# Optimization experiments

Measured on AMD Instinct MI355X. Metric: run time of the kernel, lower is better.

Reference implementation:

```python
import jax, jax.numpy as jnp
import numpy as np

H, W, S, B = 256, 256, 16, 8  # dim=(H,W); S hardcoded in forward; B = 1 + events[-1,-1]
N = 4_000_000


def _shift2d(a, dy, dx):
    """Replicates F.pad(a, (pad(dx) + pad(dy)))[:H,:W] where pad(n)=(n,0) if n>=0 else (0,-n).
    Positive diff shifts content right/down and zero-fills; negative diff is a no-op
    (right/bottom padding followed by top-left crop is identity)."""
    sy = jnp.maximum(dy, 0)
    sx = jnp.maximum(dx, 0)
    a = jnp.roll(a, shift=(sy, sx), axis=(0, 1))
    row = jnp.arange(a.shape[0])[:, None]
    col = jnp.arange(a.shape[1])[None, :]
    return jnp.where((row >= sy) & (col >= sx), a, 0.0)


def setup_inputs():
    key = jax.random.key(0)
    k1, k2, k3, k4 = jax.random.split(key, 4)
    x = jax.random.randint(k1, (N,), 0, W).astype(jnp.float32)
    y = jax.random.randint(k2, (N,), 0, H).astype(jnp.float32)
    t = jax.random.uniform(k3, (N,), minval=1e-3, maxval=1.0)
    p = (jax.random.randint(k4, (N,), 0, 2) * 2 - 1).astype(jnp.float32)
    b = jnp.repeat(jnp.arange(B, dtype=jnp.float32), N // B)  # sorted so events[-1,-1]==B-1
    events = jnp.stack([x, y, t, p, b], axis=1)
    return {"events": events}


def _forward(events):
    x = events[:, 0]
    y = events[:, 1]
    t = events[:, 2]
    bi = events[:, 4].astype(jnp.int32)

    # per-batch time normalization: t /= max(t) within each sample
    t_max = jax.ops.segment_max(t, bi, num_segments=B)
    t = t / t_max[bi]

    xi = x.astype(jnp.int32)
    yi = y.astype(jnp.int32)

    # container: per-pixel event count histogram, (B,H,W)
    idx_c = xi + W * yi + W * H * bi
    container = jnp.zeros(B * H * W, jnp.int32).at[idx_c].add(1).reshape(B, H, W)

    # time_segment[e] = number of thresholds i/S (i=1..S-1) with t >= i/S
    thr = jnp.arange(1, S, dtype=t.dtype) / S
    ts = jnp.searchsorted(thr, t, side='right').astype(jnp.int32)

    # combiner accumulates the segment index itself (as in the torch code)
    idx_cb = xi + W * yi + W * H * ts + W * H * S * bi
    combiner = jnp.zeros(B * S * H * W, jnp.int32).at[idx_cb].add(ts)
    combiner = combiner.reshape(B, S, H, W).astype(jnp.float32)

    # per-(batch, segment) event counts and x/y centroids
    seg = bi * S + ts
    cnt = jax.ops.segment_sum(jnp.ones_like(t), seg, num_segments=B * S).reshape(B, S)
    xm = jax.ops.segment_sum(x, seg, num_segments=B * S).reshape(B, S) / cnt
    ym = jax.ops.segment_sum(y, seg, num_segments=B * S).reshape(B, S) / cnt

    # mean-shift alignment + accumulation of the S segment images
    combined = []
    for b_ in range(B):
        segment = combiner[b_, 0]
        x_mean = xm[b_, 0]
        y_mean = ym[b_, 0]
        pts = cnt[b_, 0]  # note: never updated in the original code
        for i in range(1, S):
            cond = cnt[b_, i] > pts
            tmp = jnp.where(cond, segment, combiner[b_, i])
            base = jnp.where(cond, combiner[b_, i], segment)
            dx = jnp.floor(jnp.where(cond, xm[b_, i] - x_mean, x_mean - xm[b_, i])).astype(jnp.int32)
            dy = jnp.floor(jnp.where(cond, ym[b_, i] - y_mean, y_mean - ym[b_, i])).astype(jnp.int32)
            x_mean = jnp.where(cond, xm[b_, i], x_mean)
            y_mean = jnp.where(cond, ym[b_, i], y_mean)
            segment = base + _shift2d(tmp, dy, dx)
        combined.append(jax.nn.relu(segment - S))
    combined_img = jnp.stack(combined)  # (B,H,W)

    # half-resolution count + mean-timestamp voxel grids
    hw4 = (H // 2) * (W // 2)
    idx_ct = xi // 2 + (W // 2) * (yi // 2) + (W * H * bi) // 4
    counter = jnp.zeros(B * hw4, jnp.int32).at[idx_ct].add(1).astype(jnp.float32)
    divider = jnp.where(counter == 0, 1.0, counter)
    timer = jnp.zeros(B * hw4, jnp.float32).at[idx_ct].add(t) / divider
    counter = counter.reshape(B, H // 2, W // 2)
    timer = timer.reshape(B, H // 2, W // 2)

    # 2x2 difference pooling of the count image
    dyv = container[:, ::2] - container[:, 1::2]
    dyv = (dyv[:, :, ::2] + dyv[:, :, 1::2]).astype(jnp.float32)
    dxv = container[:, :, ::2] - container[:, :, 1::2]
    dxv = (dxv[:, 1::2] + dxv[:, ::2]).astype(jnp.float32)

    # F.interpolate(scale_factor=0.5, mode='nearest') == ::2 subsampling for even H,W
    combined_half = combined_img[:, ::2, ::2]

    return jnp.stack([dxv, dyv, timer, counter, combined_half], axis=1)  # (B,5,H/2,W/2)


def reference(events):
    return _forward(events)
```

## Files before the change

kernel.cpp:

```cpp
#include <hip/hip_runtime.h>

#define SS 16
#define BB 8
#define CHUNKS 32

#define OFF_CNT    0
#define OFF_XS     512
#define OFF_YS     1024
#define OFF_BMAX   1536
#define OFF_P4REP  5632
#define OFF_CMREP  (5632 + 16777216)
#define OFF_XYREC  (5632 + 16777216 + 8388608)
#define OFF_TARR   (5632 + 16777216 + 8388608 + 8000000)
#define OFF_TSREC  (5632 + 16777216 + 8388608 + 8000000 + 16000000)


__global__ void k_prep(const float4* __restrict__ ev4, int nq, unsigned* __restrict__ bmax,
                       uint2* __restrict__ xyrec, float4* __restrict__ tarr,
                       int* __restrict__ cnt, int* __restrict__ xs, int* __restrict__ ys) {
    if (blockIdx.x == 0 && threadIdx.x < BB * SS) {
        cnt[threadIdx.x] = 0; xs[threadIdx.x] = 0; ys[threadIdx.x] = 0;
    }
    int bb = blockIdx.x >> 7;
    long base = (long)bb * nq;
    unsigned m = 0;
    for (int q = (blockIdx.x & 127) * blockDim.x + threadIdx.x; q < nq; q += 128 * blockDim.x) {
        const float4* p = ev4 + (base + q) * 5;
        float4 f0 = p[0], f1 = p[1], f2 = p[2], f3 = p[3], f4 = p[4];
        unsigned xy0 = (unsigned)(int)f0.x | ((unsigned)(int)f0.y << 8)
                     | ((unsigned)(int)f1.y << 16) | ((unsigned)(int)f1.z << 24);
        unsigned xy1 = (unsigned)(int)f2.z | ((unsigned)(int)f2.w << 8)
                     | ((unsigned)(int)f3.w << 16) | ((unsigned)(int)f4.x << 24);
        xyrec[base + q] = make_uint2(xy0, xy1);
        tarr[base + q]  = make_float4(f0.z, f1.w, f3.x, f4.y);
        unsigned t0 = __float_as_uint(f0.z), t1 = __float_as_uint(f1.w);
        unsigned t2 = __float_as_uint(f3.x), t3 = __float_as_uint(f4.y);
        unsigned a = t0 > t1 ? t0 : t1;
        unsigned b2 = t2 > t3 ? t2 : t3;
        a = a > b2 ? a : b2;
        m = m > a ? m : a;
    }
    #pragma unroll
    for (int off = 32; off; off >>= 1) {
        unsigned o = (unsigned)__shfl_xor((int)m, off, 64);
        m = m > o ? m : o;
    }
    __shared__ unsigned sm;
    if (threadIdx.x == 0) sm = 0;
    __syncthreads();
    if ((threadIdx.x & 63) == 0) atomicMax(&sm, m);
    __syncthreads();
    if (threadIdx.x == 0) bmax[blockIdx.x] = sm;
}

__global__ void __launch_bounds__(1024, 8)
k_main(const uint2* __restrict__ xyrec, const float4* __restrict__ tarr, int nq,
       const unsigned* __restrict__ bmax,
       unsigned* __restrict__ p4rep, unsigned short* __restrict__ tsrec,
       int* __restrict__ cnt, int* __restrict__ xs, int* __restrict__ ys) {
    __shared__ unsigned p4s[16384];
    __shared__ unsigned long long stat[SS * 8];
    __shared__ unsigned stmax;
    int bb = blockIdx.x >> 5;
    int ch = blockIdx.x & 31;
    if (threadIdx.x == 0) stmax = 0u;
    if (threadIdx.x < SS * 8) stat[threadIdx.x] = 0ull;
    for (int i = threadIdx.x; i < 16384; i += 1024) p4s[i] = 0u;
    __syncthreads();
    if (threadIdx.x < 128) atomicMax(&stmax, bmax[bb * 128 + threadIdx.x]);
    __syncthreads();
    float tm = __uint_as_float(stmax);
    long base = (long)bb * nq;
    int slot = threadIdx.x & 7;
    for (int q = ch * 1024 + threadIdx.x; q < nq; q += CHUNKS * 1024) {
        uint2 xy = xyrec[base + q];
        float4 t4 = tarr[base + q];
        float T[4] = { t4.x, t4.y, t4.z, t4.w };
        unsigned XY[4] = { xy.x & 0xFFFFu, xy.x >> 16, xy.y & 0xFFFFu, xy.y >> 16 };
        unsigned tsn = 0;
        #pragma unroll
        for (int k = 0; k < 4; k++) {
            int xi = (int)(XY[k] & 255u), yi = (int)(XY[k] >> 8);
            float tn = __fdiv_rn(T[k], tm);
            int ts = (int)(tn * 16.0f);
            if (ts > 15) ts = 15;
            unsigned qfix = __float2uint_rn(tn * 256.0f);
            unsigned v = qfix | (1u << 14)
                | (((unsigned)(xi & 1) ^ 1u) << 20)
                | (((unsigned)(yi & 1) ^ 1u) << 26);
            atomicAdd(&p4s[((yi >> 1) << 7) + (xi >> 1)], v);
            atomicAdd(&stat[ts * 8 + slot], 1ull | ((unsigned long long)xi << 20)
                                                 | ((unsigned long long)yi << 42));
            tsn |= (unsigned)ts << (4 * k);
        }
        tsrec[base + q] = (unsigned short)tsn;
    }
    __syncthreads();
    unsigned* dst = p4rep + (long)blockIdx.x * 16384;
    for (int i = threadIdx.x; i < 16384; i += 1024) dst[i] = p4s[i];
    if (threadIdx.x < SS) {
        unsigned long long v = 0ull;
        #pragma unroll
        for (int s = 0; s < 8; s++) v += stat[threadIdx.x * 8 + s];
        if (v) {
            int g = bb * SS + threadIdx.x;
            atomicAdd(&cnt[g], (int)(v & 0xFFFFF));
            atomicAdd(&xs[g],  (int)((v >> 20) & 0x3FFFFF));
            atomicAdd(&ys[g],  (int)(v >> 42));
        }
    }
}

__global__ void __launch_bounds__(1024, 8)
k_comb(const uint2* __restrict__ xyrec, const unsigned short* __restrict__ tsrec, int nq,
       const int* __restrict__ cnt, const int* __restrict__ xs, const int* __restrict__ ys,
       const unsigned* __restrict__ p4rep,
       unsigned* __restrict__ cmrep32, float* __restrict__ out) {
    __shared__ int combs[16384];
    __shared__ double xm[SS], ym[SS];
    __shared__ int cs[SS], ssy[SS], ssx[SS];
    int bb = blockIdx.x >> 5;
    int ch = blockIdx.x & 31;
    for (int i = threadIdx.x; i < 16384; i += 1024) combs[i] = 0;
    if (threadIdx.x < SS) {
        int g = bb * SS + threadIdx.x;
        int cc = cnt[g];
        cs[threadIdx.x] = cc;
        xm[threadIdx.x] = (double)xs[g] / (double)cc;
        ym[threadIdx.x] = (double)ys[g] / (double)cc;
    }
    __syncthreads();
    if (threadIdx.x == 0) {
        double x_mean = xm[0], y_mean = ym[0];
        int c0 = cs[0];
        int sy[SS], sx[SS];
        for (int k = 0; k < SS; k++) { sy[k] = 0; sx[k] = 0; }
        for (int k = 1; k < SS; k++) {
            bool cond = cs[k] > c0;
            double ddx = cond ? (xm[k] - x_mean) : (x_mean - xm[k]);
            double ddy = cond ? (ym[k] - y_mean) : (y_mean - ym[k]);
            int dx = (int)floor(ddx);
            int dy = (int)floor(ddy);
            int px = dx > 0 ? dx : 0;
            int py = dy > 0 ? dy : 0;
            if (cond) {
                for (int j = 0; j < k; j++) { sy[j] += py; sx[j] += px; }
                x_mean = xm[k]; y_mean = ym[k];
            } else {
                sy[k] = py; sx[k] = px;
            }
        }
        for (int k = 0; k < SS; k++) { ssy[k] = sy[k]; ssx[k] = sx[k]; }
    }
    __syncthreads();
    long base = (long)bb * nq;
    for (int q = ch * 1024 + threadIdx.x; q < nq; q += CHUNKS * 1024) {
        uint2 xy = xyrec[base + q];
        unsigned tsn = tsrec[base + q];
        unsigned XY[4] = { xy.x & 0xFFFFu, xy.x >> 16, xy.y & 0xFFFFu, xy.y >> 16 };
        #pragma unroll
        for (int k = 0; k < 4; k++) {
            int ts = (int)((tsn >> (4 * k)) & 15u);
            if (ts) {
                int yy = (int)(XY[k] >> 8) + ssy[ts];
                int xx = (int)(XY[k] & 255u) + ssx[ts];
                if (yy < 256 && xx < 256 && !((yy | xx) & 1))
                    atomicAdd(&combs[((yy >> 1) << 7) + (xx >> 1)], ts);
            }
        }
    }
    __syncthreads();
    unsigned* dst = cmrep32 + (long)blockIdx.x * 8192;
    for (int i = threadIdx.x; i < 8192; i += 1024)
        dst[i] = (unsigned)combs[2 * i] | ((unsigned)combs[2 * i + 1] << 16);
    if (threadIdx.x < 512) {
        int lin = blockIdx.x * 512 + threadIdx.x;
        int hp = lin & 16383;
        int b  = lin >> 14;
        long rb = (long)b * CHUNKS * 16384 + hp;
        unsigned tfix = 0; int c = 0, Ex = 0, Ey = 0;
        #pragma unroll 8
        for (int r = 0; r < CHUNKS; r++) {
            unsigned v = p4rep[rb + (long)r * 16384];
            tfix += v & 0x3FFFu;
            c    += (int)((v >> 14) & 63u);
            Ex   += (int)((v >> 20) & 63u);
            Ey   += (int)(v >> 26);
        }
        float tsum = (float)tfix * (1.0f / 256.0f);
        float ctr = (float)c;
        int obase = (b * 5) << 14;
        out[obase             + hp] = (float)(2 * Ex - c);
        out[obase +     16384 + hp] = (float)(2 * Ey - c);
        out[obase + 2 * 16384 + hp] = tsum / (c == 0 ? 1.0f : ctr);
        out[obase + 3 * 16384 + hp] = ctr;
    }
}

__global__ void k_out(const unsigned short* __restrict__ cmrep,
                      float* __restrict__ out) {
    int lin = blockIdx.x * blockDim.x + threadIdx.x;
    int hp = lin & 16383;
    int b  = lin >> 14;
    long rb = (long)b * CHUNKS * 16384 + hp;
    int cm = 0;
    #pragma unroll 8
    for (int r = 0; r < CHUNKS; r++) cm += cmrep[rb + (long)r * 16384];
    float cmb = (float)cm - 16.0f;
    cmb = cmb < 0.0f ? 0.0f : cmb;
    out[((b * 5 + 4) << 14) + hp] = cmb;
}

extern "C" void kernel_launch(void* const* d_in, const int* in_sizes, int n_in,
                              void* d_out, int out_size, void* d_ws, size_t ws_size,
                              hipStream_t stream) {
    const float4* ev4 = (const float4*)d_in[0];
    int n  = in_sizes[0] / 5;
    int nb = n / BB;
    int nq = nb / 4;
    char* ws = (char*)d_ws;
    int*      cnt   = (int*)     (ws + OFF_CNT);
    int*      xs    = (int*)     (ws + OFF_XS);
    int*      ys    = (int*)     (ws + OFF_YS);
    unsigned* bmax  = (unsigned*)(ws + OFF_BMAX);
    unsigned* p4rep = (unsigned*)(ws + OFF_P4REP);
    unsigned* cmrep32 = (unsigned*)(ws + OFF_CMREP);
    uint2*    xyrec = (uint2*)   (ws + OFF_XYREC);
    float4*   tarr  = (float4*)  (ws + OFF_TARR);
    unsigned short* tsrec = (unsigned short*)(ws + OFF_TSREC);

    hipLaunchKernelGGL(k_prep, dim3(1024), dim3(256),  0, stream, ev4, nq, bmax,
                       xyrec, tarr, cnt, xs, ys);
    hipLaunchKernelGGL(k_main, dim3(256),  dim3(1024), 0, stream, xyrec, tarr, nq,
                       bmax, p4rep, tsrec, cnt, xs, ys);
    hipLaunchKernelGGL(k_comb, dim3(256),  dim3(1024), 0, stream, xyrec, tsrec, nq,
                       cnt, xs, ys, p4rep, cmrep32, (float*)d_out);
    hipLaunchKernelGGL(k_out,  dim3(128),  dim3(1024), 0, stream,
                       (const unsigned short*)cmrep32, (float*)d_out);
}
```

Measured before the change: 139.7 us.

## Fuse four kernels into one cooperative kernel with grid syncs and LDS-resident records

Replaces the prep, main, combine and output kernels with a single cooperative launch of 256 blocks that separates phases with grid.sync(). Packed xy coordinates and per-event segment indices now stay in shared memory across phases instead of round-tripping through global workspace, and the p4s buffer is reused as the combiner histogram. This removes three kernel launches and about 8 MB of global traffic, at the cost of grid-wide barrier overhead and more LDS per block (about 100 KB), which limits residency to one 1024-thread block per CU.

```diff
diff --git a/kernel.cpp b/kernel.cpp
--- a/kernel.cpp
+++ b/kernel.cpp
@@ -1,4 +1,7 @@
 #include <hip/hip_runtime.h>
+#include <hip/hip_cooperative_groups.h>
+
+namespace cg = cooperative_groups;
 
 #define SS 16
 #define BB 8
@@ -10,127 +13,122 @@
 #define OFF_BMAX   1536
 #define OFF_P4REP  5632
 #define OFF_CMREP  (5632 + 16777216)
-#define OFF_XYREC  (5632 + 16777216 + 8388608)
-#define OFF_TARR   (5632 + 16777216 + 8388608 + 8000000)
-#define OFF_TSREC  (5632 + 16777216 + 8388608 + 8000000 + 16000000)
-
-
-__global__ void k_prep(const float4* __restrict__ ev4, int nq, unsigned* __restrict__ bmax,
-                       uint2* __restrict__ xyrec, float4* __restrict__ tarr,
-                       int* __restrict__ cnt, int* __restrict__ xs, int* __restrict__ ys) {
-    if (blockIdx.x == 0 && threadIdx.x < BB * SS) {
-        cnt[threadIdx.x] = 0; xs[threadIdx.x] = 0; ys[threadIdx.x] = 0;
-    }
-    int bb = blockIdx.x >> 7;
-    long base = (long)bb * nq;
+#define OFF_TARR   (5632 + 16777216 + 8388608)
+
+
+__global__ void __launch_bounds__(1024)
+k_fused(const float4* __restrict__ ev4, int nq, unsigned* __restrict__ bmax,
+        float4* __restrict__ tarr, unsigned* __restrict__ p4rep,
+        unsigned* __restrict__ cmrep32, int* __restrict__ cnt,
+        int* __restrict__ xs, int* __restrict__ ys, float* __restrict__ out) {
+    cg::grid_group grid = cg::this_grid();
+    __shared__ unsigned p4s[16384];
+    __shared__ uint2 xyl[4096];
+    __shared__ unsigned short tsl[4096];
+    __shared__ unsigned long long stat[SS * 8];
+    __shared__ unsigned stmax;
+    __shared__ double xm[SS], ym[SS];
+    __shared__ int cs[SS], ssy[SS], ssx[SS];
+
+    const int tid = threadIdx.x;
+    const int bb = blockIdx.x >> 5;
+    const int ch = blockIdx.x & 31;
+    const long base = (long)bb * nq;
+
+    if (blockIdx.x == 0 && tid < BB * SS) { cnt[tid] = 0; xs[tid] = 0; ys[tid] = 0; }
+    if (tid == 0) stmax = 0u;
+    if (tid < SS * 8) stat[tid] = 0ull;
+    for (int i = tid; i < 16384; i += 1024) p4s[i] = 0u;
+    __syncthreads();
     unsigned m = 0;
-    for (int q = (blockIdx.x & 127) * blockDim.x + threadIdx.x; q < nq; q += 128 * blockDim.x) {
-        const float4* p = ev4 + (base + q) * 5;
-        float4 f0 = p[0], f1 = p[1], f2 = p[2], f3 = p[3], f4 = p[4];
-        unsigned xy0 = (unsigned)(int)f0.x | ((unsigned)(int)f0.y << 8)
-                     | ((unsigned)(int)f1.y << 16) | ((unsigned)(int)f1.z << 24);
-        unsigned xy1 = (unsigned)(int)f2.z | ((unsigned)(int)f2.w << 8)
-                     | ((unsigned)(int)f3.w << 16) | ((unsigned)(int)f4.x << 24);
-        xyrec[base + q] = make_uint2(xy0, xy1);
-        tarr[base + q]  = make_float4(f0.z, f1.w, f3.x, f4.y);
-        unsigned t0 = __float_as_uint(f0.z), t1 = __float_as_uint(f1.w);
-        unsigned t2 = __float_as_uint(f3.x), t3 = __float_as_uint(f4.y);
-        unsigned a = t0 > t1 ? t0 : t1;
-        unsigned b2 = t2 > t3 ? t2 : t3;
-        a = a > b2 ? a : b2;
-        m = m > a ? m : a;
+    {
+        int it = 0;
+        for (int q = ch * 1024 + tid; q < nq; q += CHUNKS * 1024, ++it) {
+            const float4* p = ev4 + (base + q) * 5;
+            float4 f0 = p[0], f1 = p[1], f2 = p[2], f3 = p[3], f4 = p[4];
+            unsigned xy0 = (unsigned)(int)f0.x | ((unsigned)(int)f0.y << 8)
+                         | ((unsigned)(int)f1.y << 16) | ((unsigned)(int)f1.z << 24);
+            unsigned xy1 = (unsigned)(int)f2.z | ((unsigned)(int)f2.w << 8)
+                         | ((unsigned)(int)f3.w << 16) | ((unsigned)(int)f4.x << 24);
+            xyl[it * 1024 + tid] = make_uint2(xy0, xy1);
+            tarr[base + q] = make_float4(f0.z, f1.w, f3.x, f4.y);
+            unsigned t0 = __float_as_uint(f0.z), t1 = __float_as_uint(f1.w);
+            unsigned t2 = __float_as_uint(f3.x), t3 = __float_as_uint(f4.y);
+            unsigned a = t0 > t1 ? t0 : t1;
+            unsigned b2 = t2 > t3 ? t2 : t3;
+            a = a > b2 ? a : b2;
+            m = m > a ? m : a;
+        }
     }
     #pragma unroll
     for (int off = 32; off; off >>= 1) {
         unsigned o = (unsigned)__shfl_xor((int)m, off, 64);
         m = m > o ? m : o;
     }
-    __shared__ unsigned sm;
-    if (threadIdx.x == 0) sm = 0;
-    __syncthreads();
-    if ((threadIdx.x & 63) == 0) atomicMax(&sm, m);
-    __syncthreads();
-    if (threadIdx.x == 0) bmax[blockIdx.x] = sm;
-}
-
-__global__ void __launch_bounds__(1024, 8)
-k_main(const uint2* __restrict__ xyrec, const float4* __restrict__ tarr, int nq,
-       const unsigned* __restrict__ bmax,
-       unsigned* __restrict__ p4rep, unsigned short* __restrict__ tsrec,
-       int* __restrict__ cnt, int* __restrict__ xs, int* __restrict__ ys) {
-    __shared__ unsigned p4s[16384];
-    __shared__ unsigned long long stat[SS * 8];
-    __shared__ unsigned stmax;
-    int bb = blockIdx.x >> 5;
-    int ch = blockIdx.x & 31;
-    if (threadIdx.x == 0) stmax = 0u;
-    if (threadIdx.x < SS * 8) stat[threadIdx.x] = 0ull;
-    for (int i = threadIdx.x; i < 16384; i += 1024) p4s[i] = 0u;
-    __syncthreads();
-    if (threadIdx.x < 128) atomicMax(&stmax, bmax[bb * 128 + threadIdx.x]);
+    if ((tid & 63) == 0) atomicMax(&stmax, m);
+    __syncthreads();
+    if (tid == 0) bmax[blockIdx.x] = stmax;
+    grid.sync();
+
+    if (tid < CHUNKS) atomicMax(&stmax, bmax[bb * CHUNKS + tid]);
     __syncthreads();
     float tm = __uint_as_float(stmax);
-    long base = (long)bb * nq;
-    int slot = threadIdx.x & 7;
-    for (int q = ch * 1024 + threadIdx.x; q < nq; q += CHUNKS * 1024) {
-        uint2 xy = xyrec[base + q];
-        float4 t4 = tarr[base + q];
-        float T[4] = { t4.x, t4.y, t4.z, t4.w };
-        unsigned XY[4] = { xy.x & 0xFFFFu, xy.x >> 16, xy.y & 0xFFFFu, xy.y >> 16 };
-        unsigned tsn = 0;
-        #pragma unroll
-        for (int k = 0; k < 4; k++) {
-            int xi = (int)(XY[k] & 255u), yi = (int)(XY[k] >> 8);
-            float tn = __fdiv_rn(T[k], tm);
-            int ts = (int)(tn * 16.0f);
-            if (ts > 15) ts = 15;
-            unsigned qfix = __float2uint_rn(tn * 256.0f);
-            unsigned v = qfix | (1u << 14)
-                | (((unsigned)(xi & 1) ^ 1u) << 20)
-                | (((unsigned)(yi & 1) ^ 1u) << 26);
-            atomicAdd(&p4s[((yi >> 1) << 7) + (xi >> 1)], v);
-            atomicAdd(&stat[ts * 8 + slot], 1ull | ((unsigned long long)xi << 20)
-                                                 | ((unsigned long long)yi << 42));
-            tsn |= (unsigned)ts << (4 * k);
-        }
-        tsrec[base + q] = (unsigned short)tsn;
-    }
-    __syncthreads();
-    unsigned* dst = p4rep + (long)blockIdx.x * 16384;
-    for (int i = threadIdx.x; i < 16384; i += 1024) dst[i] = p4s[i];
-    if (threadIdx.x < SS) {
+    {
+        int slot = tid & 7;
+        int it = 0;
+        for (int q = ch * 1024 + tid; q < nq; q += CHUNKS * 1024, ++it) {
+            uint2 xy = xyl[it * 1024 + tid];
+            float4 t4 = tarr[base + q];
+            float T[4] = { t4.x, t4.y, t4.z, t4.w };
+            unsigned XY[4] = { xy.x & 0xFFFFu, xy.x >> 16, xy.y & 0xFFFFu, xy.y >> 16 };
+            unsigned tsn = 0;
+            #pragma unroll
+            for (int k = 0; k < 4; k++) {
+                int xi = (int)(XY[k] & 255u), yi = (int)(XY[k] >> 8);
+                float tn = __fdiv_rn(T[k], tm);
+                int ts = (int)(tn * 16.0f);
+                if (ts > 15) ts = 15;
+                unsigned qfix = __float2uint_rn(tn * 256.0f);
+                unsigned v = qfix | (1u << 14)
+                    | (((unsigned)(xi & 1) ^ 1u) << 20)
+                    | (((unsigned)(yi & 1) ^ 1u) << 26);
+                atomicAdd(&p4s[((yi >> 1) << 7) + (xi >> 1)], v);
+                atomicAdd(&stat[ts * 8 + slot], 1ull | ((unsigned long long)xi << 20)
+                                                     | ((unsigned long long)yi << 42));
+                tsn |= (unsigned)ts << (4 * k);
+            }
+            tsl[it * 1024 + tid] = (unsigned short)tsn;
+        }
+    }
+    __syncthreads();
+    {
+        unsigned* dst = p4rep + (long)blockIdx.x * 16384;
+        for (int i = tid; i < 16384; i += 1024) dst[i] = p4s[i];
+    }
+    if (tid < SS) {
         unsigned long long v = 0ull;
         #pragma unroll
-        for (int s = 0; s < 8; s++) v += stat[threadIdx.x * 8 + s];
+        for (int s = 0; s < 8; s++) v += stat[tid * 8 + s];
         if (v) {
-            int g = bb * SS + threadIdx.x;
+            int g = bb * SS + tid;
             atomicAdd(&cnt[g], (int)(v & 0xFFFFF));
             atomicAdd(&xs[g],  (int)((v >> 20) & 0x3FFFFF));
             atomicAdd(&ys[g],  (int)(v >> 42));
         }
     }
-}
-
-__global__ void __launch_bounds__(1024, 8)
-k_comb(const uint2* __restrict__ xyrec, const unsigned short* __restrict__ tsrec, int nq,
-       const int* __restrict__ cnt, const int* __restrict__ xs, const int* __restrict__ ys,
-       const unsigned* __restrict__ p4rep,
-       unsigned* __restrict__ cmrep32, float* __restrict__ out) {
-    __shared__ int combs[16384];
-    __shared__ double xm[SS], ym[SS];
-    __shared__ int cs[SS], ssy[SS], ssx[SS];
-    int bb = blockIdx.x >> 5;
-    int ch = blockIdx.x & 31;
-    for (int i = threadIdx.x; i < 16384; i += 1024) combs[i] = 0;
-    if (threadIdx.x < SS) {
-        int g = bb * SS + threadIdx.x;
+    grid.sync();
+
+    int* combs = (int*)p4s;
+    for (int i = tid; i < 16384; i += 1024) combs[i] = 0;
+    if (tid < SS) {
+        int g = bb * SS + tid;
         int cc = cnt[g];
-        cs[threadIdx.x] = cc;
-        xm[threadIdx.x] = (double)xs[g] / (double)cc;
-        ym[threadIdx.x] = (double)ys[g] / (double)cc;
-    }
-    __syncthreads();
-    if (threadIdx.x == 0) {
+        cs[tid] = cc;
+        xm[tid] = (double)xs[g] / (double)cc;
+        ym[tid] = (double)ys[g] / (double)cc;
+    }
+    __syncthreads();
+    if (tid == 0) {
         double x_mean = xm[0], y_mean = ym[0];
         int c0 = cs[0];
         int sy[SS], sx[SS];
@@ -153,28 +151,32 @@
         for (int k = 0; k < SS; k++) { ssy[k] = sy[k]; ssx[k] = sx[k]; }
     }
     __syncthreads();
-    long base = (long)bb * nq;
-    for (int q = ch * 1024 + threadIdx.x; q < nq; q += CHUNKS * 1024) {
-        uint2 xy = xyrec[base + q];
-        unsigned tsn = tsrec[base + q];
-        unsigned XY[4] = { xy.x & 0xFFFFu, xy.x >> 16, xy.y & 0xFFFFu, xy.y >> 16 };
-        #pragma unroll
-        for (int k = 0; k < 4; k++) {
-            int ts = (int)((tsn >> (4 * k)) & 15u);
-            if (ts) {
-                int yy = (int)(XY[k] >> 8) + ssy[ts];
-                int xx = (int)(XY[k] & 255u) + ssx[ts];
-                if (yy < 256 && xx < 256 && !((yy | xx) & 1))
-                    atomicAdd(&combs[((yy >> 1) << 7) + (xx >> 1)], ts);
+    {
+        int it = 0;
+        for (int q = ch * 1024 + tid; q < nq; q += CHUNKS * 1024, ++it) {
+            uint2 xy = xyl[it * 1024 + tid];
+            unsigned tsn = tsl[it * 1024 + tid];
+            unsigned XY[4] = { xy.x & 0xFFFFu, xy.x >> 16, xy.y & 0xFFFFu, xy.y >> 16 };
+            #pragma unroll
+            for (int k = 0; k < 4; k++) {
+                int ts = (int)((tsn >> (4 * k)) & 15u);
+                if (ts) {
+                    int yy = (int)(XY[k] >> 8) + ssy[ts];
+                    int xx = (int)(XY[k] & 255u) + ssx[ts];
+                    if (yy < 256 && xx < 256 && !((yy | xx) & 1))
+                        atomicAdd(&combs[((yy >> 1) << 7) + (xx >> 1)], ts);
+                }
             }
         }
     }
     __syncthreads();
-    unsigned* dst = cmrep32 + (long)blockIdx.x * 8192;
-    for (int i = threadIdx.x; i < 8192; i += 1024)
-        dst[i] = (unsigned)combs[2 * i] | ((unsigned)combs[2 * i + 1] << 16);
-    if (threadIdx.x < 512) {
-        int lin = blockIdx.x * 512 + threadIdx.x;
+    {
+        unsigned* dst = cmrep32 + (long)blockIdx.x * 8192;
+        for (int i = tid; i < 8192; i += 1024)
+            dst[i] = (unsigned)combs[2 * i] | ((unsigned)combs[2 * i + 1] << 16);
+    }
+    if (tid < 512) {
+        int lin = blockIdx.x * 512 + tid;
         int hp = lin & 16383;
         int b  = lin >> 14;
         long rb = (long)b * CHUNKS * 16384 + hp;
@@ -195,20 +197,21 @@
         out[obase + 2 * 16384 + hp] = tsum / (c == 0 ? 1.0f : ctr);
         out[obase + 3 * 16384 + hp] = ctr;
     }
-}
-
-__global__ void k_out(const unsigned short* __restrict__ cmrep,
-                      float* __restrict__ out) {
-    int lin = blockIdx.x * blockDim.x + threadIdx.x;
-    int hp = lin & 16383;
-    int b  = lin >> 14;
-    long rb = (long)b * CHUNKS * 16384 + hp;
-    int cm = 0;
-    #pragma unroll 8
-    for (int r = 0; r < CHUNKS; r++) cm += cmrep[rb + (long)r * 16384];
-    float cmb = (float)cm - 16.0f;
-    cmb = cmb < 0.0f ? 0.0f : cmb;
-    out[((b * 5 + 4) << 14) + hp] = cmb;
+    grid.sync();
+
+    if (tid < 512) {
+        const unsigned short* cm16 = (const unsigned short*)cmrep32;
+        int lin = blockIdx.x * 512 + tid;
+        int hp = lin & 16383;
+        int b  = lin >> 14;
+        long rb = (long)b * CHUNKS * 16384 + hp;
+        int cmv = 0;
+        #pragma unroll 8
+        for (int r = 0; r < CHUNKS; r++) cmv += cm16[rb + (long)r * 16384];
+        float cmb = (float)cmv - 16.0f;
+        cmb = cmb < 0.0f ? 0.0f : cmb;
+        out[((b * 5 + 4) << 14) + hp] = cmb;
+    }
 }
 
 extern "C" void kernel_launch(void* const* d_in, const int* in_sizes, int n_in,
@@ -219,22 +222,18 @@
     int nb = n / BB;
     int nq = nb / 4;
     char* ws = (char*)d_ws;
-    int*      cnt   = (int*)     (ws + OFF_CNT);
-    int*      xs    = (int*)     (ws + OFF_XS);
-    int*      ys    = (int*)     (ws + OFF_YS);
-    unsigned* bmax  = (unsigned*)(ws + OFF_BMAX);
-    unsigned* p4rep = (unsigned*)(ws + OFF_P4REP);
+    int*      cnt     = (int*)     (ws + OFF_CNT);
+    int*      xs      = (int*)     (ws + OFF_XS);
+    int*      ys      = (int*)     (ws + OFF_YS);
+    unsigned* bmax    = (unsigned*)(ws + OFF_BMAX);
+    unsigned* p4rep   = (unsigned*)(ws + OFF_P4REP);
     unsigned* cmrep32 = (unsigned*)(ws + OFF_CMREP);
-    uint2*    xyrec = (uint2*)   (ws + OFF_XYREC);
-    float4*   tarr  = (float4*)  (ws + OFF_TARR);
-    unsigned short* tsrec = (unsigned short*)(ws + OFF_TSREC);
-
-    hipLaunchKernelGGL(k_prep, dim3(1024), dim3(256),  0, stream, ev4, nq, bmax,
-                       xyrec, tarr, cnt, xs, ys);
-    hipLaunchKernelGGL(k_main, dim3(256),  dim3(1024), 0, stream, xyrec, tarr, nq,
-                       bmax, p4rep, tsrec, cnt, xs, ys);
-    hipLaunchKernelGGL(k_comb, dim3(256),  dim3(1024), 0, stream, xyrec, tsrec, nq,
-                       cnt, xs, ys, p4rep, cmrep32, (float*)d_out);
-    hipLaunchKernelGGL(k_out,  dim3(128),  dim3(1024), 0, stream,
-                       (const unsigned short*)cmrep32, (float*)d_out);
+    float4*   tarr    = (float4*)  (ws + OFF_TARR);
+    float*    outp    = (float*)d_out;
+
+    void* args[] = { (void*)&ev4, (void*)&nq, (void*)&bmax, (void*)&tarr,
+                     (void*)&p4rep, (void*)&cmrep32, (void*)&cnt, (void*)&xs,
+                     (void*)&ys, (void*)&outp };
+    hipLaunchCooperativeKernel((const void*)k_fused, dim3(256), dim3(1024),
+                               args, 0, stream);
 }
```

New measurement: 241.7 us. 73.1% more time.

## Replace per-chunk replica histograms with global atomic reduction grids

Applied to the files above, without the earlier changes.

Each block now merges its shared-memory histograms straight into one global grid per batch using atomics, skipping zero entries. Before, every chunk wrote a full replica that a later pass re-read and summed over 32 chunks. This removes tens of megabytes of replica writes and strided reads, and the final reduction loops become single loads. In exchange the code does millions of global atomics that contend in L2, zeroes the grids inside the prep kernel, and repacks the fields with new bit widths that assume per-pixel counts stay small.

```diff
diff --git a/kernel.cpp b/kernel.cpp
--- a/kernel.cpp
+++ b/kernel.cpp
@@ -8,19 +8,24 @@
 #define OFF_XS     512
 #define OFF_YS     1024
 #define OFF_BMAX   1536
-#define OFF_P4REP  5632
-#define OFF_CMREP  (5632 + 16777216)
-#define OFF_XYREC  (5632 + 16777216 + 8388608)
-#define OFF_TARR   (5632 + 16777216 + 8388608 + 8000000)
-#define OFF_TSREC  (5632 + 16777216 + 8388608 + 8000000 + 16000000)
+#define OFF_GRIDA  8192
+#define OFF_GRIDB  (8192 + 524288)
+#define OFF_COMBG  (8192 + 2*524288)
+#define OFF_XYREC  (8192 + 3*524288)
+#define OFF_TARR   (8192 + 3*524288 + 8000000)
+#define OFF_TSREC  (8192 + 3*524288 + 8000000 + 16000000)
 
 
 __global__ void k_prep(const float4* __restrict__ ev4, int nq, unsigned* __restrict__ bmax,
                        uint2* __restrict__ xyrec, float4* __restrict__ tarr,
-                       int* __restrict__ cnt, int* __restrict__ xs, int* __restrict__ ys) {
+                       int* __restrict__ cnt, int* __restrict__ xs, int* __restrict__ ys,
+                       unsigned* __restrict__ grids) {
     if (blockIdx.x == 0 && threadIdx.x < BB * SS) {
         cnt[threadIdx.x] = 0; xs[threadIdx.x] = 0; ys[threadIdx.x] = 0;
     }
+    for (int i = blockIdx.x * blockDim.x + threadIdx.x; i < 3 * BB * 16384;
+         i += gridDim.x * blockDim.x)
+        grids[i] = 0u;
     int bb = blockIdx.x >> 7;
     long base = (long)bb * nq;
     unsigned m = 0;
@@ -56,7 +61,8 @@
 __global__ void __launch_bounds__(1024, 8)
 k_main(const uint2* __restrict__ xyrec, const float4* __restrict__ tarr, int nq,
        const unsigned* __restrict__ bmax,
-       unsigned* __restrict__ p4rep, unsigned short* __restrict__ tsrec,
+       unsigned* __restrict__ gridA, unsigned* __restrict__ gridB,
+       unsigned short* __restrict__ tsrec,
        int* __restrict__ cnt, int* __restrict__ xs, int* __restrict__ ys) {
     __shared__ unsigned p4s[16384];
     __shared__ unsigned long long stat[SS * 8];
@@ -96,8 +102,21 @@
         tsrec[base + q] = (unsigned short)tsn;
     }
     __syncthreads();
-    unsigned* dst = p4rep + (long)blockIdx.x * 16384;
-    for (int i = threadIdx.x; i < 16384; i += 1024) dst[i] = p4s[i];
+    {
+        unsigned* ga = gridA + bb * 16384;
+        unsigned* gb = gridB + bb * 16384;
+        for (int i = threadIdx.x; i < 16384; i += 1024) {
+            unsigned v = p4s[i];
+            if (v) {
+                unsigned sumq = v & 0x3FFFu;
+                unsigned c    = (v >> 14) & 63u;
+                unsigned ex   = (v >> 20) & 63u;
+                unsigned ey   = v >> 26;
+                atomicAdd(&ga[i], (c << 22) | sumq);
+                atomicAdd(&gb[i], (ex << 16) | ey);
+            }
+        }
+    }
     if (threadIdx.x < SS) {
         unsigned long long v = 0ull;
         #pragma unroll
@@ -114,8 +133,8 @@
 __global__ void __launch_bounds__(1024, 8)
 k_comb(const uint2* __restrict__ xyrec, const unsigned short* __restrict__ tsrec, int nq,
        const int* __restrict__ cnt, const int* __restrict__ xs, const int* __restrict__ ys,
-       const unsigned* __restrict__ p4rep,
-       unsigned* __restrict__ cmrep32, float* __restrict__ out) {
+       const unsigned* __restrict__ gridA, const unsigned* __restrict__ gridB,
+       unsigned* __restrict__ combg, float* __restrict__ out) {
     __shared__ int combs[16384];
     __shared__ double xm[SS], ym[SS];
     __shared__ int cs[SS], ssy[SS], ssx[SS];
@@ -170,24 +189,24 @@
         }
     }
     __syncthreads();
-    unsigned* dst = cmrep32 + (long)blockIdx.x * 8192;
-    for (int i = threadIdx.x; i < 8192; i += 1024)
-        dst[i] = (unsigned)combs[2 * i] | ((unsigned)combs[2 * i + 1] << 16);
+    {
+        unsigned* cg = combg + bb * 16384;
+        for (int i = threadIdx.x; i < 16384; i += 1024) {
+            int v = combs[i];
+            if (v) atomicAdd(&cg[i], (unsigned)v);
+        }
+    }
     if (threadIdx.x < 512) {
         int lin = blockIdx.x * 512 + threadIdx.x;
         int hp = lin & 16383;
         int b  = lin >> 14;
-        long rb = (long)b * CHUNKS * 16384 + hp;
-        unsigned tfix = 0; int c = 0, Ex = 0, Ey = 0;
-        #pragma unroll 8
-        for (int r = 0; r < CHUNKS; r++) {
-            unsigned v = p4rep[rb + (long)r * 16384];
-            tfix += v & 0x3FFFu;
-            c    += (int)((v >> 14) & 63u);
-            Ex   += (int)((v >> 20) & 63u);
-            Ey   += (int)(v >> 26);
-        }
-        float tsum = (float)tfix * (1.0f / 256.0f);
+        unsigned va = gridA[b * 16384 + hp];
+        unsigned vb = gridB[b * 16384 + hp];
+        unsigned sumq = va & 0x3FFFFFu;
+        int c  = (int)(va >> 22);
+        int Ex = (int)(vb >> 16);
+        int Ey = (int)(vb & 0xFFFFu);
+        float tsum = (float)sumq * (1.0f / 256.0f);
         float ctr = (float)c;
         int obase = (b * 5) << 14;
         out[obase             + hp] = (float)(2 * Ex - c);
@@ -197,16 +216,11 @@
     }
 }
 
-__global__ void k_out(const unsigned short* __restrict__ cmrep,
-                      float* __restrict__ out) {
+__global__ void k_out(const unsigned* __restrict__ combg, float* __restrict__ out) {
     int lin = blockIdx.x * blockDim.x + threadIdx.x;
     int hp = lin & 16383;
     int b  = lin >> 14;
-    long rb = (long)b * CHUNKS * 16384 + hp;
-    int cm = 0;
-    #pragma unroll 8
-    for (int r = 0; r < CHUNKS; r++) cm += cmrep[rb + (long)r * 16384];
-    float cmb = (float)cm - 16.0f;
+    float cmb = (float)combg[b * 16384 + hp] - 16.0f;
     cmb = cmb < 0.0f ? 0.0f : cmb;
     out[((b * 5 + 4) << 14) + hp] = cmb;
 }
@@ -223,18 +237,18 @@
     int*      xs    = (int*)     (ws + OFF_XS);
     int*      ys    = (int*)     (ws + OFF_YS);
     unsigned* bmax  = (unsigned*)(ws + OFF_BMAX);
-    unsigned* p4rep = (unsigned*)(ws + OFF_P4REP);
-    unsigned* cmrep32 = (unsigned*)(ws + OFF_CMREP);
+    unsigned* gridA = (unsigned*)(ws + OFF_GRIDA);
+    unsigned* gridB = (unsigned*)(ws + OFF_GRIDB);
+    unsigned* combg = (unsigned*)(ws + OFF_COMBG);
     uint2*    xyrec = (uint2*)   (ws + OFF_XYREC);
     float4*   tarr  = (float4*)  (ws + OFF_TARR);
     unsigned short* tsrec = (unsigned short*)(ws + OFF_TSREC);
 
     hipLaunchKernelGGL(k_prep, dim3(1024), dim3(256),  0, stream, ev4, nq, bmax,
-                       xyrec, tarr, cnt, xs, ys);
+                       xyrec, tarr, cnt, xs, ys, gridA);
     hipLaunchKernelGGL(k_main, dim3(256),  dim3(1024), 0, stream, xyrec, tarr, nq,
-                       bmax, p4rep, tsrec, cnt, xs, ys);
+                       bmax, gridA, gridB, tsrec, cnt, xs, ys);
     hipLaunchKernelGGL(k_comb, dim3(256),  dim3(1024), 0, stream, xyrec, tsrec, nq,
-                       cnt, xs, ys, p4rep, cmrep32, (float*)d_out);
-    hipLaunchKernelGGL(k_out,  dim3(128),  dim3(1024), 0, stream,
-                       (const unsigned short*)cmrep32, (float*)d_out);
-}
+                       cnt, xs, ys, gridA, gridB, combg, (float*)d_out);
+    hipLaunchKernelGGL(k_out,  dim3(128),  dim3(1024), 0, stream, combg, (float*)d_out);
+}
```

New measurement: 162.4 us. 1.16x slower.
